# Kernel optimization log

Hardware: AMD Instinct MI355X
Metric: run time of the kernel (lower is better)

Reference implementation:

```python
import math
import jax, jax.numpy as jnp
import numpy as np

B, L, D = 8, 4096, 512
FACTOR = 5


def setup_inputs() -> dict:
    key = jax.random.key(0)
    kq, kk, kv = jax.random.split(key, 3)
    q = jax.random.normal(kq, (B, L, D), dtype=jnp.float32)
    k = jax.random.normal(kk, (B, L, D), dtype=jnp.float32)
    v = jax.random.normal(kv, (B, L, D), dtype=jnp.float32)
    return {"q": q, "k": k, "v": v}


def reference(q, k, v):
    # ProbSparse attention (sparse=True branch, L_Q > 1)
    L_Q = q.shape[1]
    scale = q.shape[-1] ** -0.5
    # scores: [B, L_Q, L_K]
    scores = jnp.einsum('bqd,bkd->bqk', q, k) * scale
    # sparsity measure M = max - mean over keys: [B, L_Q]
    M = scores.max(axis=-1) - scores.mean(axis=-1)
    u = max(1, int(FACTOR * math.log(L_Q + 1)))
    u = min(u, L_Q)  # static python int (u = 41 here)
    _, top_idx = jax.lax.top_k(M, u)  # [B, u]
    # gather top-u query rows of scores, softmax over keys (row-wise softmax
    # commutes with row selection, so this matches softmax-then-gather)
    scores_top = jnp.take_along_axis(scores, top_idx[:, :, None], axis=1)  # [B, u, L_K]
    attn = jax.nn.softmax(scores_top, axis=-1)
    out_top = jnp.einsum('buk,bkd->bud', attn, v)  # [B, u, D]
    # non-selected queries receive the mean value
    v_mean = jnp.broadcast_to(v.mean(axis=1, keepdims=True), v.shape)  # [B, L, D]
    b_idx = jnp.arange(q.shape[0])[:, None]  # [B, 1]
    out = v_mean.at[b_idx, top_idx].set(out_top)
    return out
```

## Files before the change

kernel.cpp:

```cpp
#include <hip/hip_runtime.h>
#include <math.h>

#define B_ 8
#define L_ 4096
#define D_ 512
#define U_ 41
#define NSL 16

static constexpr float SCALE = 0.044194173824159216f;

typedef __attribute__((ext_vector_type(8))) short bf16x8;
typedef __attribute__((ext_vector_type(4))) float f32x4;
typedef unsigned int uint;


__global__ __launch_bounds__(512) void kSums1(const float* __restrict__ k,
                                              const float* __restrict__ v,
                                              float* __restrict__ partk,
                                              float* __restrict__ partv) {
  const int s = blockIdx.x;
  const int b = blockIdx.y;
  const int d = threadIdx.x;
  const int rows = L_ / NSL;
  const size_t base = ((size_t)b * L_ + (size_t)s * rows) * D_ + d;
  float ks = 0.f, vs = 0.f;
  for (int l = 0; l < rows; ++l) {
    ks += k[base + (size_t)l * D_];
    vs += v[base + (size_t)l * D_];
  }
  partk[(b * NSL + s) * D_ + d] = ks;
  partv[(b * NSL + s) * D_ + d] = vs;
}

__global__ __launch_bounds__(512) void kSums2(const float* __restrict__ partk,
                                              const float* __restrict__ partv,
                                              float* __restrict__ ksum,
                                              float* __restrict__ vmean) {
  const int b = blockIdx.x;
  const int d = threadIdx.x;
  float ks = 0.f, vs = 0.f;
  for (int s = 0; s < NSL; ++s) {
    ks += partk[(b * NSL + s) * D_ + d];
    vs += partv[(b * NSL + s) * D_ + d];
  }
  ksum[b * D_ + d] = ks;
  vmean[b * D_ + d] = vs * (1.f / L_);
}

__global__ __launch_bounds__(256) void kMeanM(const float* __restrict__ q,
                                              const float* __restrict__ ksum,
                                              const float* __restrict__ pmax,
                                              float* __restrict__ M) {
  __shared__ float ks[D_];
  const int gid = blockIdx.x * 256 + threadIdx.x;
  const int b = gid >> 12;
  for (int i = threadIdx.x; i < D_; i += 256) ks[i] = ksum[b * D_ + i];
  __syncthreads();
  const float* qp = q + (size_t)gid * D_;
  float acc = 0.f;
  for (int i = 0; i < D_; i += 4) {
    float4 t = *(const float4*)(qp + i);
    acc += t.x * ks[i] + t.y * ks[i + 1] + t.z * ks[i + 2] + t.w * ks[i + 3];
  }
  const float rowmax = fmaxf(pmax[gid], pmax[B_ * L_ + gid]);
  M[gid] = SCALE * (rowmax - acc * (1.f / L_));
}

__global__ __launch_bounds__(256) void kTopK3(const float* __restrict__ M,
                                              int* __restrict__ topidx) {
  __shared__ float wv[2][4];
  __shared__ int wi[2][4];
  const int b = blockIdx.x;
  const int tid = threadIdx.x;
  const int wave = tid >> 6, lane = tid & 63;
  float v[16];
#pragma unroll
  for (int j = 0; j < 16; ++j) v[j] = M[b * L_ + tid + j * 256];
  float bv = v[0];
  int bj = 0;
#pragma unroll
  for (int j = 1; j < 16; ++j)
    if (v[j] > bv) { bv = v[j]; bj = j; }
  int bi = tid + bj * 256;

  for (int it = 0; it < U_; ++it) {
    float rv = bv;
    int ri = bi;
#pragma unroll
    for (int off = 1; off < 64; off <<= 1) {
      float ov = __shfl_xor(rv, off);
      int oi = __shfl_xor(ri, off);
      if (ov > rv || (ov == rv && oi < ri)) { rv = ov; ri = oi; }
    }
    const int par = it & 1;
    if (lane == 0) { wv[par][wave] = rv; wi[par][wave] = ri; }
    __syncthreads();
    float gv = wv[par][0];
    int gi = wi[par][0];
#pragma unroll
    for (int w = 1; w < 4; ++w) {
      float ov = wv[par][w];
      int oi = wi[par][w];
      if (ov > gv || (ov == gv && oi < gi)) { gv = ov; gi = oi; }
    }
    if (tid == 0) topidx[b * U_ + it] = gi;
    if (gi == bi) {
      const int jb = gi >> 8;
#pragma unroll
      for (int j = 0; j < 16; ++j)
        if (j == jb) v[j] = -3.4e38f;
      bv = v[0];
      bj = 0;
#pragma unroll
      for (int j = 1; j < 16; ++j)
        if (v[j] > bv) { bv = v[j]; bj = j; }
      bi = tid + bj * 256;
    }
  }
}

__global__ __launch_bounds__(256) void kFill(const float* __restrict__ vmean,
                                             float* __restrict__ out) {
  const int g = blockIdx.x * 256 + threadIdx.x;
  const int d4 = g & 127;
  const int bl = g >> 7;
  const int b = bl >> 12;
  ((float4*)out)[g] = ((const float4*)vmean)[b * 128 + d4];
}

__device__ inline uint bf16_rne_bits(float x) {
  uint u = __builtin_bit_cast(uint, x);
  return (u + 0x7FFFu + ((u >> 16) & 1u)) >> 16;
}
__device__ inline float bits_to_f32(uint hi16) {
  return __builtin_bit_cast(float, hi16 << 16);
}

__global__ __launch_bounds__(256) void kConvert(const float* __restrict__ src,
                                                unsigned char* __restrict__ dhi,
                                                unsigned char* __restrict__ dlo) {
  const int cid = blockIdx.x * 256 + threadIdx.x;
  const int c16 = cid & 7;
  const int row = (cid >> 3) & 127;
  const int dsi = (cid >> 10) & 7;
  const int rt = (cid >> 13) & 31;
  const int b = cid >> 18;
  const int l = rt * 128 + row;
  const int d = dsi * 64 + c16 * 8;
  const float* sp = src + ((size_t)(b * L_ + l) * D_ + d);
  float x[8];
  *(float4*)(x) = *(const float4*)sp;
  *(float4*)(x + 4) = *(const float4*)(sp + 4);
  uint hw[4], lw[4];
#pragma unroll
  for (int p = 0; p < 4; ++p) {
    float a = x[2 * p], c = x[2 * p + 1];
    uint ha = bf16_rne_bits(a), hc = bf16_rne_bits(c);
    float ra = a - bits_to_f32(ha);
    float rc = c - bits_to_f32(hc);
    uint la = bf16_rne_bits(ra), lc = bf16_rne_bits(rc);
    hw[p] = ha | (hc << 16);
    lw[p] = la | (lc << 16);
  }
  const size_t dstByte = ((size_t)(cid >> 3) << 7) +
                         (uint)((c16 << 4) ^ ((row & 7) << 4));
  *(uint4*)(dhi + dstByte) = make_uint4(hw[0], hw[1], hw[2], hw[3]);
  *(uint4*)(dlo + dstByte) = make_uint4(lw[0], lw[1], lw[2], lw[3]);
}

__device__ __forceinline__ void gload16(const unsigned char* g, unsigned char* l) {
  __builtin_amdgcn_global_load_lds(
      (const __attribute__((address_space(1))) unsigned int*)(g),
      (__attribute__((address_space(3))) unsigned int*)(l), 16, 0, 0);
}

__global__ __launch_bounds__(256, 1) void kRowMaxC(const unsigned char* __restrict__ qhi,
                                                   const unsigned char* __restrict__ qlo,
                                                   const unsigned char* __restrict__ khi,
                                                   const unsigned char* __restrict__ klo,
                                                   float* __restrict__ pmax) {
  __shared__ unsigned char lds[131072];

  const int wg = blockIdx.x;
  const int swz = (wg & 7) * 64 + (wg >> 3);
  const int qt = swz & 31;
  const int b = (swz >> 5) & 7;
  const int kh = swz >> 8;

  const int tid = threadIdx.x;
  const int lane = tid & 63;
  const int wave = tid >> 6;
  const int wq = wave >> 1, wk = wave & 1;

  const unsigned char* qhB = qhi + ((size_t)((b * 32 + qt) * 8)) * 16384;
  const unsigned char* qlB = qlo + ((size_t)((b * 32 + qt) * 8)) * 16384;
  const size_t kbase = ((size_t)((b * 32 + kh * 16) * 8)) * 16384;
  const unsigned char* khB = khi + kbase;
  const unsigned char* klB = klo + kbase;

  const size_t lof = (size_t)tid * 16;

  auto STAGE = [&](int s, unsigned char* buf) {
    const int dsi = s & 7;
    const size_t qof = (size_t)dsi * 16384 + lof;
    const size_t kof = (size_t)s * 16384 + lof;
#pragma unroll
    for (int i = 0; i < 4; ++i) {
      gload16(qhB + qof + i * 4096, buf + lof + i * 4096);
      gload16(qlB + qof + i * 4096, buf + 16384 + lof + i * 4096);
      gload16(khB + kof + i * 4096, buf + 32768 + lof + i * 4096);
      gload16(klB + kof + i * 4096, buf + 49152 + lof + i * 4096);
    }
  };

  float rmax[4][4];
  f32x4 acc[4][4];
#pragma unroll
  for (int i = 0; i < 4; ++i)
#pragma unroll
    for (int j = 0; j < 4; ++j) {
      rmax[i][j] = -3.4e38f;
#pragma unroll
      for (int e = 0; e < 4; ++e) acc[i][j][e] = 0.f;
    }

  auto PHASE = [&](int s, const unsigned char* bufR, unsigned char* bufW) {
    __syncthreads();
    if (s < 127) STAGE(s + 1, bufW);
#pragma unroll
    for (int h = 0; h < 2; ++h) {
      const int rbyte = h * 64 + ((lane >> 4) << 4);
      bf16x8 aH[4], aL[4], bH[4], bL[4];
#pragma unroll
      for (int f = 0; f < 4; ++f) {
        const int qrow = wq * 64 + f * 16 + (lane & 15);
        const int krow = wk * 64 + f * 16 + (lane & 15);
        const int qoff = qrow * 128 + (rbyte ^ ((qrow & 7) << 4));
        const int koff = krow * 128 + (rbyte ^ ((krow & 7) << 4));
        aH[f] = *(const bf16x8*)(bufR + qoff);
        aL[f] = *(const bf16x8*)(bufR + 16384 + qoff);
        bH[f] = *(const bf16x8*)(bufR + 32768 + koff);
        bL[f] = *(const bf16x8*)(bufR + 49152 + koff);
      }
#pragma unroll
      for (int mf = 0; mf < 4; ++mf)
#pragma unroll
        for (int nf = 0; nf < 4; ++nf) {
          acc[mf][nf] = __builtin_amdgcn_mfma_f32_16x16x32_bf16(aH[mf], bH[nf], acc[mf][nf], 0, 0, 0);
          acc[mf][nf] = __builtin_amdgcn_mfma_f32_16x16x32_bf16(aH[mf], bL[nf], acc[mf][nf], 0, 0, 0);
          acc[mf][nf] = __builtin_amdgcn_mfma_f32_16x16x32_bf16(aL[mf], bH[nf], acc[mf][nf], 0, 0, 0);
        }
    }
    if ((s & 7) == 7) {
#pragma unroll
      for (int mf = 0; mf < 4; ++mf)
#pragma unroll
        for (int r = 0; r < 4; ++r) {
          float m = fmaxf(fmaxf(acc[mf][0][r], acc[mf][1][r]),
                          fmaxf(acc[mf][2][r], acc[mf][3][r]));
          rmax[mf][r] = fmaxf(rmax[mf][r], m);
#pragma unroll
          for (int nf = 0; nf < 4; ++nf) acc[mf][nf][r] = 0.f;
        }
    }
  };

  STAGE(0, lds);
  for (int s = 0; s < 128; s += 2) {
    PHASE(s, lds, lds + 65536);
    PHASE(s + 1, lds + 65536, lds);
  }

#pragma unroll
  for (int mf = 0; mf < 4; ++mf)
#pragma unroll
    for (int r = 0; r < 4; ++r) {
      float v = rmax[mf][r];
#pragma unroll
      for (int off = 1; off < 16; off <<= 1) v = fmaxf(v, __shfl_xor(v, off));
      rmax[mf][r] = v;
    }

  __syncthreads();
  float* red = (float*)lds;
  if ((lane & 15) == 0) {
#pragma unroll
    for (int mf = 0; mf < 4; ++mf)
#pragma unroll
      for (int r = 0; r < 4; ++r) {
        const int rowl = wq * 64 + mf * 16 + ((lane >> 4) << 2) + r;
        red[wk * 128 + rowl] = rmax[mf][r];
      }
  }
  __syncthreads();
  if (tid < 128) {
    pmax[(size_t)kh * B_ * L_ + (size_t)b * L_ + qt * 128 + tid] =
        fmaxf(red[tid], red[128 + tid]);
  }
}


__global__ __launch_bounds__(64) void kGatherQ(const float* __restrict__ q,
                                               const int* __restrict__ topidx,
                                               unsigned char* __restrict__ qselhi,
                                               unsigned char* __restrict__ qsello) {
  const int j = blockIdx.x;
  const int b = blockIdx.y;
  const int lane = threadIdx.x;
  const int dsi = lane >> 3;
  const int c16 = lane & 7;
  float x[8] = {0.f, 0.f, 0.f, 0.f, 0.f, 0.f, 0.f, 0.f};
  if (j < U_) {
    const int row = topidx[b * U_ + j];
    const float* sp = q + ((size_t)(b * L_ + row)) * D_ + dsi * 64 + c16 * 8;
    *(float4*)(x) = *(const float4*)sp;
    *(float4*)(x + 4) = *(const float4*)(sp + 4);
  }
  uint hw[4], lw[4];
#pragma unroll
  for (int p = 0; p < 4; ++p) {
    float a = x[2 * p], c = x[2 * p + 1];
    uint ha = bf16_rne_bits(a), hc = bf16_rne_bits(c);
    float ra = a - bits_to_f32(ha);
    float rc = c - bits_to_f32(hc);
    uint la = bf16_rne_bits(ra), lc = bf16_rne_bits(rc);
    hw[p] = ha | (hc << 16);
    lw[p] = la | (lc << 16);
  }
  const size_t dstByte = ((size_t)((b * 8 + dsi) * 64 + j)) * 128 +
                         (uint)((c16 << 4) ^ ((j & 7) << 4));
  *(uint4*)(qselhi + dstByte) = make_uint4(hw[0], hw[1], hw[2], hw[3]);
  *(uint4*)(qsello + dstByte) = make_uint4(lw[0], lw[1], lw[2], lw[3]);
}

__global__ __launch_bounds__(256) void kSelScoresM(const unsigned char* __restrict__ qselhi,
                                                   const unsigned char* __restrict__ qsello,
                                                   const unsigned char* __restrict__ khi,
                                                   const unsigned char* __restrict__ klo,
                                                   float* __restrict__ P) {
  __shared__ unsigned char lds[49152];
  unsigned char* ldsQhi = lds;
  unsigned char* ldsQlo = lds + 8192;
  unsigned char* ldsKhi = lds + 16384;
  unsigned char* ldsKlo = lds + 32768;

  const int kc = blockIdx.x;
  const int b = blockIdx.y;
  const int tid = threadIdx.x;
  const int lane = tid & 63;
  const int wave = tid >> 6;
  const int wq = wave >> 1, wk = wave & 1;

  const size_t ktb = ((size_t)((b * 32 + kc) * 8)) * 16384;
  const unsigned char* khB = khi + ktb;
  const unsigned char* klB = klo + ktb;
  const size_t qb = ((size_t)b * 8) * 8192;
  const unsigned char* qhB = qselhi + qb;
  const unsigned char* qlB = qsello + qb;

  f32x4 acc[2][4];
#pragma unroll
  for (int i = 0; i < 2; ++i)
#pragma unroll
    for (int j = 0; j < 4; ++j)
#pragma unroll
      for (int e = 0; e < 4; ++e) acc[i][j][e] = 0.f;

  for (int dsi = 0; dsi < 8; ++dsi) {
    __syncthreads();
    {
      const size_t qof = (size_t)dsi * 8192 + (size_t)tid * 16;
      const size_t kof = (size_t)dsi * 16384 + (size_t)tid * 16;
      const size_t lof = (size_t)tid * 16;
#pragma unroll
      for (int i = 0; i < 2; ++i) {
        gload16(qhB + qof + i * 4096, ldsQhi + lof + i * 4096);
        gload16(qlB + qof + i * 4096, ldsQlo + lof + i * 4096);
      }
#pragma unroll
      for (int i = 0; i < 4; ++i) {
        gload16(khB + kof + i * 4096, ldsKhi + lof + i * 4096);
        gload16(klB + kof + i * 4096, ldsKlo + lof + i * 4096);
      }
    }
    __syncthreads();

#pragma unroll
    for (int h = 0; h < 2; ++h) {
      const int rbyte = h * 64 + ((lane >> 4) << 4);
      bf16x8 aH[2], aL[2], bH[4], bL[4];
#pragma unroll
      for (int f = 0; f < 2; ++f) {
        const int qrow = wq * 32 + f * 16 + (lane & 15);
        const int qoff = qrow * 128 + (rbyte ^ ((qrow & 7) << 4));
        aH[f] = *(const bf16x8*)(ldsQhi + qoff);
        aL[f] = *(const bf16x8*)(ldsQlo + qoff);
      }
#pragma unroll
      for (int f = 0; f < 4; ++f) {
        const int krow = wk * 64 + f * 16 + (lane & 15);
        const int koff = krow * 128 + (rbyte ^ ((krow & 7) << 4));
        bH[f] = *(const bf16x8*)(ldsKhi + koff);
        bL[f] = *(const bf16x8*)(ldsKlo + koff);
      }
#pragma unroll
      for (int mf = 0; mf < 2; ++mf)
#pragma unroll
        for (int nf = 0; nf < 4; ++nf) {
          acc[mf][nf] = __builtin_amdgcn_mfma_f32_16x16x32_bf16(aH[mf], bH[nf], acc[mf][nf], 0, 0, 0);
          acc[mf][nf] = __builtin_amdgcn_mfma_f32_16x16x32_bf16(aH[mf], bL[nf], acc[mf][nf], 0, 0, 0);
          acc[mf][nf] = __builtin_amdgcn_mfma_f32_16x16x32_bf16(aL[mf], bH[nf], acc[mf][nf], 0, 0, 0);
        }
    }
  }

#pragma unroll
  for (int mf = 0; mf < 2; ++mf)
#pragma unroll
    for (int nf = 0; nf < 4; ++nf)
#pragma unroll
      for (int r = 0; r < 4; ++r) {
        const int row = wq * 32 + mf * 16 + ((lane >> 4) << 2) + r;
        const int key = kc * 128 + wk * 64 + nf * 16 + (lane & 15);
        if (row < U_)
          P[((size_t)(b * U_ + row)) * L_ + key] = acc[mf][nf][r];
      }
}

__global__ __launch_bounds__(256) void kSoftmaxP(float* __restrict__ P) {
  __shared__ float red[256];
  const int j = blockIdx.x, b = blockIdx.y;
  float* row = P + ((size_t)(b * U_ + j)) * L_;
  const int tid = threadIdx.x;
  float v[16];
  float mx = -3.4e38f;
#pragma unroll
  for (int i = 0; i < 16; ++i) {
    v[i] = row[tid + i * 256];
    mx = fmaxf(mx, v[i]);
  }
  red[tid] = mx;
  __syncthreads();
  for (int s = 128; s > 0; s >>= 1) {
    if (tid < s) red[tid] = fmaxf(red[tid], red[tid + s]);
    __syncthreads();
  }
  mx = red[0];
  __syncthreads();
  float sum = 0.f;
#pragma unroll
  for (int i = 0; i < 16; ++i) {
    float e = expf((v[i] - mx) * SCALE);
    v[i] = e;
    sum += e;
  }
  red[tid] = sum;
  __syncthreads();
  for (int s = 128; s > 0; s >>= 1) {
    if (tid < s) red[tid] += red[tid + s];
    __syncthreads();
  }
  const float inv = 1.f / red[0];
#pragma unroll
  for (int i = 0; i < 16; ++i) row[tid + i * 256] = v[i] * inv;
}

__global__ __launch_bounds__(256) void kPV(const float* __restrict__ P,
                                           const float* __restrict__ v,
                                           float* __restrict__ partial) {
  __shared__ float plds[41 * 128];
  const int kc = blockIdx.x;
  const int dc = blockIdx.y;
  const int b = blockIdx.z;
  const int tid = threadIdx.x;
  const int trow = tid >> 7, dcol = tid & 127;
  float acc[U_];
#pragma unroll
  for (int j = 0; j < U_; ++j) acc[j] = 0.f;

  for (int sub = 0; sub < 4; ++sub) {
    const int key0 = kc * 512 + sub * 128;
    __syncthreads();
    for (int idx = tid; idx < U_ * 128; idx += 256)
      plds[idx] = P[((size_t)(b * U_ + (idx >> 7))) * L_ + key0 + (idx & 127)];
    __syncthreads();
    const float* vp = v + ((size_t)(b * L_ + key0 + trow * 64)) * D_ + dc * 128 + dcol;
    float vv[64];
#pragma unroll
    for (int kk = 0; kk < 64; ++kk) vv[kk] = vp[(size_t)kk * D_];
#pragma unroll
    for (int j = 0; j < U_; ++j) {
      const float4* pr = (const float4*)&plds[j * 128 + trow * 64];
      float a = acc[j];
#pragma unroll
      for (int q4 = 0; q4 < 16; ++q4) {
        float4 p4 = pr[q4];
        a = fmaf(p4.x, vv[q4 * 4 + 0], a);
        a = fmaf(p4.y, vv[q4 * 4 + 1], a);
        a = fmaf(p4.z, vv[q4 * 4 + 2], a);
        a = fmaf(p4.w, vv[q4 * 4 + 3], a);
      }
      acc[j] = a;
    }
  }
  float* pp = partial + ((size_t)((b * 4 + dc) * 16 + kc * 2 + trow)) * (U_ * 128) + dcol;
#pragma unroll
  for (int j = 0; j < U_; ++j) pp[j * 128] = acc[j];
}

__global__ __launch_bounds__(256) void kPVout(const float* __restrict__ partial,
                                              const int* __restrict__ topidx,
                                              float* __restrict__ out) {
  const int j = blockIdx.x, b = blockIdx.y;
  const int tid = threadIdx.x;
  const int l = topidx[b * U_ + j];
#pragma unroll
  for (int h = 0; h < 2; ++h) {
    const int d = tid + h * 256;
    const int dc = d >> 7, dcol = d & 127;
    float s = 0.f;
#pragma unroll
    for (int part = 0; part < 16; ++part)
      s += partial[((size_t)((b * 4 + dc) * 16 + part)) * (U_ * 128) + j * 128 + dcol];
    out[((size_t)(b * L_ + l)) * D_ + d] = s;
  }
}


__device__ inline void stageHalfRow(const float* __restrict__ src,
                                    char* hiBase, char* loBase,
                                    int row, int shalf) {
  const int sw = (row & 7) << 4;
  char* hp = hiBase + row * 128;
  char* lp = loBase + row * 128;
#pragma unroll
  for (int g = 0; g < 4; ++g) {
    f32x4 x0 = *(const f32x4*)(src + g * 8);
    f32x4 x1 = *(const f32x4*)(src + g * 8 + 4);
    float x[8] = {x0.x, x0.y, x0.z, x0.w, x1.x, x1.y, x1.z, x1.w};
    uint hw[4], lw[4];
#pragma unroll
    for (int p = 0; p < 4; ++p) {
      float a = x[2 * p], c = x[2 * p + 1];
      uint ha = bf16_rne_bits(a), hc = bf16_rne_bits(c);
      float ra = a - bits_to_f32(ha);
      float rc = c - bits_to_f32(hc);
      uint la = bf16_rne_bits(ra), lc = bf16_rne_bits(rc);
      hw[p] = ha | (hc << 16);
      lw[p] = la | (lc << 16);
    }
    const int off = (shalf * 64 + g * 16) ^ sw;
    *(uint4*)(hp + off) = make_uint4(hw[0], hw[1], hw[2], hw[3]);
    *(uint4*)(lp + off) = make_uint4(lw[0], lw[1], lw[2], lw[3]);
  }
}

__global__ __launch_bounds__(256, 2) void kRowMaxM(const float* __restrict__ q,
                                                   const float* __restrict__ k,
                                                   float* __restrict__ pmax) {
  __shared__ char lds[65536];
  __shared__ float red[256];
  char* ldsQhi = lds;
  char* ldsQlo = lds + 16384;
  char* ldsKhi = lds + 32768;
  char* ldsKlo = lds + 49152;

  const int b = blockIdx.y;
  const int qbase = blockIdx.x * 128;
  const int kh = blockIdx.z;
  const int tid = threadIdx.x;
  const int lane = tid & 63;
  const int wave = tid >> 6;
  const int wq = wave >> 1, wk = wave & 1;
  const int srow = tid >> 1;
  const int shalf = tid & 1;

  const float* qrow_base = q + ((size_t)b * L_ + qbase + srow) * D_ + shalf * 32;
  const float* krow_base = k + ((size_t)b * L_ + kh * 2048 + srow) * D_ + shalf * 32;

  float rmax[4][4];
#pragma unroll
  for (int i = 0; i < 4; ++i)
#pragma unroll
    for (int j = 0; j < 4; ++j) rmax[i][j] = -3.4e38f;

  for (int kt = 0; kt < 16; ++kt) {
    f32x4 acc[4][4];
#pragma unroll
    for (int i = 0; i < 4; ++i)
#pragma unroll
      for (int j = 0; j < 4; ++j)
#pragma unroll
        for (int e = 0; e < 4; ++e) acc[i][j][e] = 0.f;

    for (int dsi = 0; dsi < 8; ++dsi) {
      __syncthreads();
      stageHalfRow(qrow_base + dsi * 64, ldsQhi, ldsQlo, srow, shalf);
      stageHalfRow(krow_base + (size_t)kt * 128 * D_ + dsi * 64, ldsKhi, ldsKlo, srow, shalf);
      __syncthreads();

#pragma unroll
      for (int h = 0; h < 2; ++h) {
        const int rbyte = h * 64 + ((lane >> 4) << 4);
        bf16x8 aH[4], aL[4], bH[4], bL[4];
#pragma unroll
        for (int f = 0; f < 4; ++f) {
          const int qrow = wq * 64 + f * 16 + (lane & 15);
          const int krow = wk * 64 + f * 16 + (lane & 15);
          const int qoff = qrow * 128 + (rbyte ^ ((qrow & 7) << 4));
          const int koff = krow * 128 + (rbyte ^ ((krow & 7) << 4));
          aH[f] = *(const bf16x8*)(ldsQhi + qoff);
          aL[f] = *(const bf16x8*)(ldsQlo + qoff);
          bH[f] = *(const bf16x8*)(ldsKhi + koff);
          bL[f] = *(const bf16x8*)(ldsKlo + koff);
        }
#pragma unroll
        for (int mf = 0; mf < 4; ++mf)
#pragma unroll
          for (int nf = 0; nf < 4; ++nf) {
            acc[mf][nf] = __builtin_amdgcn_mfma_f32_16x16x32_bf16(aH[mf], bH[nf], acc[mf][nf], 0, 0, 0);
            acc[mf][nf] = __builtin_amdgcn_mfma_f32_16x16x32_bf16(aH[mf], bL[nf], acc[mf][nf], 0, 0, 0);
            acc[mf][nf] = __builtin_amdgcn_mfma_f32_16x16x32_bf16(aL[mf], bH[nf], acc[mf][nf], 0, 0, 0);
          }
      }
    }
#pragma unroll
    for (int mf = 0; mf < 4; ++mf)
#pragma unroll
      for (int r = 0; r < 4; ++r) {
        float m = fmaxf(fmaxf(acc[mf][0][r], acc[mf][1][r]),
                        fmaxf(acc[mf][2][r], acc[mf][3][r]));
        rmax[mf][r] = fmaxf(rmax[mf][r], m);
      }
  }

#pragma unroll
  for (int mf = 0; mf < 4; ++mf)
#pragma unroll
    for (int r = 0; r < 4; ++r) {
      float v = rmax[mf][r];
#pragma unroll
      for (int off = 1; off < 16; off <<= 1) v = fmaxf(v, __shfl_xor(v, off));
      rmax[mf][r] = v;
    }

  if ((lane & 15) == 0) {
#pragma unroll
    for (int mf = 0; mf < 4; ++mf)
#pragma unroll
      for (int r = 0; r < 4; ++r) {
        const int rowl = wq * 64 + mf * 16 + ((lane >> 4) << 2) + r;
        red[wk * 128 + rowl] = rmax[mf][r];
      }
  }
  __syncthreads();
  if (tid < 128) {
    pmax[(size_t)kh * B_ * L_ + (size_t)b * L_ + qbase + tid] =
        fmaxf(red[tid], red[128 + tid]);
  }
}

__global__ __launch_bounds__(256) void kAttnSel(const float* __restrict__ q,
                                                const float* __restrict__ k,
                                                const float* __restrict__ v,
                                                const int* __restrict__ topidx,
                                                float* __restrict__ out) {
  __shared__ float qs[D_];
  __shared__ float sc[L_];
  __shared__ float wred[4];
  __shared__ float sred[256];
  const int b = blockIdx.y;
  const int l_sel = topidx[b * U_ + blockIdx.x];
  const int tid = threadIdx.x;
  const int wave = tid >> 6, lane = tid & 63;
  const float* qrow = q + ((size_t)b * L_ + l_sel) * D_;
  qs[tid] = qrow[tid];
  qs[tid + 256] = qrow[tid + 256];
  __syncthreads();
  float qr[8];
#pragma unroll
  for (int i = 0; i < 8; ++i) qr[i] = qs[lane * 8 + i];
  float wmax = -3.4e38f;
  for (int l = wave; l < L_; l += 4) {
    const float* kp = k + ((size_t)b * L_ + l) * D_ + lane * 8;
    float4 k0 = *(const float4*)kp;
    float4 k1 = *(const float4*)(kp + 4);
    float p = k0.x * qr[0] + k0.y * qr[1] + k0.z * qr[2] + k0.w * qr[3] +
              k1.x * qr[4] + k1.y * qr[5] + k1.z * qr[6] + k1.w * qr[7];
#pragma unroll
    for (int off = 32; off > 0; off >>= 1) p += __shfl_xor(p, off);
    if (lane == 0) sc[l] = p;
    wmax = fmaxf(wmax, p);
  }
  if (lane == 0) wred[wave] = wmax;
  __syncthreads();
  const float mx = fmaxf(fmaxf(wred[0], wred[1]), fmaxf(wred[2], wred[3]));
  float psum = 0.f;
  for (int i = tid; i < L_; i += 256) {
    float e = expf((sc[i] - mx) * SCALE);
    sc[i] = e;
    psum += e;
  }
  sred[tid] = psum;
  __syncthreads();
  for (int s = 128; s > 0; s >>= 1) {
    if (tid < s) sred[tid] += sred[tid + s];
    __syncthreads();
  }
  const float inv = 1.f / sred[0];
  float a0a = 0.f, a0b = 0.f, a1a = 0.f, a1b = 0.f;
  const float* vb = v + (size_t)b * L_ * D_;
  for (int l = 0; l < L_; l += 2) {
    float p0 = sc[l], p1 = sc[l + 1];
    const float* vp0 = vb + (size_t)l * D_;
    const float* vp1 = vp0 + D_;
    a0a = fmaf(p0, vp0[tid], a0a);
    a1a = fmaf(p0, vp0[tid + 256], a1a);
    a0b = fmaf(p1, vp1[tid], a0b);
    a1b = fmaf(p1, vp1[tid + 256], a1b);
  }
  float* orow = out + ((size_t)b * L_ + l_sel) * D_;
  orow[tid] = (a0a + a0b) * inv;
  orow[tid + 256] = (a1a + a1b) * inv;
}


extern "C" void kernel_launch(void* const* d_in, const int* in_sizes, int n_in,
                              void* d_out, int out_size, void* d_ws, size_t ws_size,
                              hipStream_t stream) {
  const float* q = (const float*)d_in[0];
  const float* k = (const float*)d_in[1];
  const float* v = (const float*)d_in[2];
  float* out = (float*)d_out;
  unsigned char* wsb = (unsigned char*)d_ws;

  const size_t NEED = 84183040;

  if (ws_size >= NEED) {
    unsigned char* qhiW = wsb;
    unsigned char* qloW = wsb + 33554432;
    float* pmax = (float*)(wsb + 67108864);
    float* Marr = (float*)(wsb + 67371008);
    float* ksum = (float*)(wsb + 67502080);
    float* vmean = (float*)(wsb + 67518464);
    int* tidx = (int*)(wsb + 67534848);
    float* partk = (float*)(wsb + 67536896);
    float* partv = (float*)(wsb + 67799040);
    float* P = (float*)(wsb + 68061184);
    float* partial = (float*)(wsb + 73435136);
    unsigned char* qselhi = (unsigned char*)partial;
    unsigned char* qsello = qselhi + 524288;
    unsigned char* khiO = (unsigned char*)d_out;
    unsigned char* kloO = khiO + 33554432;

    kConvert<<<8192, 256, 0, stream>>>(q, qhiW, qloW);
    kConvert<<<8192, 256, 0, stream>>>(k, khiO, kloO);
    kSums1<<<dim3(NSL, B_), 512, 0, stream>>>(k, v, partk, partv);
    kSums2<<<B_, 512, 0, stream>>>(partk, partv, ksum, vmean);
    kRowMaxC<<<512, 256, 0, stream>>>(qhiW, qloW, khiO, kloO, pmax);
    kMeanM<<<B_ * L_ / 256, 256, 0, stream>>>(q, ksum, pmax, Marr);
    kTopK3<<<B_, 256, 0, stream>>>(Marr, tidx);
    kGatherQ<<<dim3(64, B_), 64, 0, stream>>>(q, tidx, qselhi, qsello);
    kSelScoresM<<<dim3(32, B_), 256, 0, stream>>>(qselhi, qsello, khiO, kloO, P);
    kSoftmaxP<<<dim3(U_, B_), 256, 0, stream>>>(P);
    kFill<<<B_ * L_ * D_ / 1024, 256, 0, stream>>>(vmean, out);
    kPV<<<dim3(8, 4, B_), 256, 0, stream>>>(P, v, partial);
    kPVout<<<dim3(U_, B_), 256, 0, stream>>>(partial, tidx, out);
  } else {
    float* ws = (float*)d_ws;
    float* Marr = ws;
    float* pmax = ws + 32768;
    float* ksum = ws + 98304;
    float* vmean = ws + 102400;
    int* tidx = (int*)(ws + 106496);
    float* partk = ws + 107008;
    float* partv = ws + 107008 + B_ * NSL * D_;

    kSums1<<<dim3(NSL, B_), 512, 0, stream>>>(k, v, partk, partv);
    kSums2<<<B_, 512, 0, stream>>>(partk, partv, ksum, vmean);
    kRowMaxM<<<dim3(L_ / 128, B_, 2), 256, 0, stream>>>(q, k, pmax);
    kMeanM<<<B_ * L_ / 256, 256, 0, stream>>>(q, ksum, pmax, Marr);
    kTopK3<<<B_, 256, 0, stream>>>(Marr, tidx);
    kFill<<<B_ * L_ * D_ / 1024, 256, 0, stream>>>(vmean, out);
    kAttnSel<<<dim3(U_, B_), 256, 0, stream>>>(q, k, v, tidx, out);
  }
}
```

Before: 677.7 us.

## Fuse q·ksum into q conversion, fold M into top-k, restructure rowmax kernel

Computes the per-row q·ksum dot product inside the q bf16 split conversion, so the separate mean-score kernel no longer re-reads q. The M = max − mean computation moves into a new top-k kernel that reads pmax and qdot directly. The rowmax GEMM is restructured to reuse one 64KB LDS stage per d-slice with launch_bounds of 2 blocks per CU, replacing the double-buffered 128KB pipeline. This trades the load/compute overlap for higher occupancy. It also doubles the k/v sum slice count and compacts the workspace layout.

```diff
diff --git a/kernel.cpp b/kernel.cpp
--- a/kernel.cpp
+++ b/kernel.cpp
@@ -5,7 +5,7 @@
 #define L_ 4096
 #define D_ 512
 #define U_ 41
-#define NSL 16
+#define NSL 32
 
 static constexpr float SCALE = 0.044194173824159216f;
 
@@ -76,6 +76,63 @@
   float v[16];
 #pragma unroll
   for (int j = 0; j < 16; ++j) v[j] = M[b * L_ + tid + j * 256];
+  float bv = v[0];
+  int bj = 0;
+#pragma unroll
+  for (int j = 1; j < 16; ++j)
+    if (v[j] > bv) { bv = v[j]; bj = j; }
+  int bi = tid + bj * 256;
+
+  for (int it = 0; it < U_; ++it) {
+    float rv = bv;
+    int ri = bi;
+#pragma unroll
+    for (int off = 1; off < 64; off <<= 1) {
+      float ov = __shfl_xor(rv, off);
+      int oi = __shfl_xor(ri, off);
+      if (ov > rv || (ov == rv && oi < ri)) { rv = ov; ri = oi; }
+    }
+    const int par = it & 1;
+    if (lane == 0) { wv[par][wave] = rv; wi[par][wave] = ri; }
+    __syncthreads();
+    float gv = wv[par][0];
+    int gi = wi[par][0];
+#pragma unroll
+    for (int w = 1; w < 4; ++w) {
+      float ov = wv[par][w];
+      int oi = wi[par][w];
+      if (ov > gv || (ov == gv && oi < gi)) { gv = ov; gi = oi; }
+    }
+    if (tid == 0) topidx[b * U_ + it] = gi;
+    if (gi == bi) {
+      const int jb = gi >> 8;
+#pragma unroll
+      for (int j = 0; j < 16; ++j)
+        if (j == jb) v[j] = -3.4e38f;
+      bv = v[0];
+      bj = 0;
+#pragma unroll
+      for (int j = 1; j < 16; ++j)
+        if (v[j] > bv) { bv = v[j]; bj = j; }
+      bi = tid + bj * 256;
+    }
+  }
+}
+
+__global__ __launch_bounds__(256) void kTopK3M(const float* __restrict__ pmax,
+                                               const float* __restrict__ qdot,
+                                               int* __restrict__ topidx) {
+  __shared__ float wv[2][4];
+  __shared__ int wi[2][4];
+  const int b = blockIdx.x;
+  const int tid = threadIdx.x;
+  const int wave = tid >> 6, lane = tid & 63;
+  float v[16];
+#pragma unroll
+  for (int j = 0; j < 16; ++j) {
+    const int gid = b * L_ + tid + j * 256;
+    v[j] = SCALE * (fmaxf(pmax[gid], pmax[B_ * L_ + gid]) - qdot[gid] * (1.f / L_));
+  }
   float bv = v[0];
   int bj = 0;
 #pragma unroll
@@ -168,18 +225,76 @@
   *(uint4*)(dlo + dstByte) = make_uint4(lw[0], lw[1], lw[2], lw[3]);
 }
 
+__global__ __launch_bounds__(256) void kConvertQdot(const float* __restrict__ src,
+                                                    const float* __restrict__ ksum,
+                                                    unsigned char* __restrict__ dhi,
+                                                    unsigned char* __restrict__ dlo,
+                                                    float* __restrict__ qdot) {
+  const int cid = blockIdx.x * 256 + threadIdx.x;
+  const int c16 = cid & 7;
+  const int row = (cid >> 3) & 127;
+  const int dsi = (cid >> 10) & 7;
+  const int rt = (cid >> 13) & 31;
+  const int b = cid >> 18;
+  const int l = rt * 128 + row;
+  const int d = dsi * 64 + c16 * 8;
+  const float* sp = src + ((size_t)(b * L_ + l) * D_ + d);
+  float x[8];
+  *(float4*)(x) = *(const float4*)sp;
+  *(float4*)(x + 4) = *(const float4*)(sp + 4);
+
+  const float* kp = ksum + b * D_ + d;
+  float dot = 0.f;
+#pragma unroll
+  for (int i = 0; i < 8; ++i) dot += x[i] * kp[i];
+#pragma unroll
+  for (int off = 1; off < 8; off <<= 1) dot += __shfl_xor(dot, off);
+
+  uint hw[4], lw[4];
+#pragma unroll
+  for (int p = 0; p < 4; ++p) {
+    float a = x[2 * p], c = x[2 * p + 1];
+    uint ha = bf16_rne_bits(a), hc = bf16_rne_bits(c);
+    float ra = a - bits_to_f32(ha);
+    float rc = c - bits_to_f32(hc);
+    uint la = bf16_rne_bits(ra), lc = bf16_rne_bits(rc);
+    hw[p] = ha | (hc << 16);
+    lw[p] = la | (lc << 16);
+  }
+  const size_t dstByte = ((size_t)(cid >> 3) << 7) +
+                         (uint)((c16 << 4) ^ ((row & 7) << 4));
+  *(uint4*)(dhi + dstByte) = make_uint4(hw[0], hw[1], hw[2], hw[3]);
+  *(uint4*)(dlo + dstByte) = make_uint4(lw[0], lw[1], lw[2], lw[3]);
+  if (c16 == 0)
+    qdot[((size_t)dsi * B_ * L_) + b * L_ + l] = dot;
+}
+
+__global__ __launch_bounds__(256) void kQdotReduce(const float* __restrict__ qdotp,
+                                                   float* __restrict__ qdot) {
+  const int gid = blockIdx.x * 256 + threadIdx.x;
+  float s = 0.f;
+#pragma unroll
+  for (int i = 0; i < 8; ++i) s += qdotp[(size_t)i * B_ * L_ + gid];
+  qdot[gid] = s;
+}
+
 __device__ __forceinline__ void gload16(const unsigned char* g, unsigned char* l) {
   __builtin_amdgcn_global_load_lds(
       (const __attribute__((address_space(1))) unsigned int*)(g),
       (__attribute__((address_space(3))) unsigned int*)(l), 16, 0, 0);
 }
 
-__global__ __launch_bounds__(256, 1) void kRowMaxC(const unsigned char* __restrict__ qhi,
+__global__ __launch_bounds__(256, 2) void kRowMaxB(const unsigned char* __restrict__ qhi,
                                                    const unsigned char* __restrict__ qlo,
                                                    const unsigned char* __restrict__ khi,
                                                    const unsigned char* __restrict__ klo,
                                                    float* __restrict__ pmax) {
-  __shared__ unsigned char lds[131072];
+  __shared__ unsigned char lds[65536];
+  __shared__ float red[256];
+  unsigned char* ldsQhi = lds;
+  unsigned char* ldsQlo = lds + 16384;
+  unsigned char* ldsKhi = lds + 32768;
+  unsigned char* ldsKlo = lds + 49152;
 
   const int wg = blockIdx.x;
   const int swz = (wg & 7) * 64 + (wg >> 3);
@@ -192,83 +307,77 @@
   const int wave = tid >> 6;
   const int wq = wave >> 1, wk = wave & 1;
 
-  const unsigned char* qhB = qhi + ((size_t)((b * 32 + qt) * 8)) * 16384;
-  const unsigned char* qlB = qlo + ((size_t)((b * 32 + qt) * 8)) * 16384;
-  const size_t kbase = ((size_t)((b * 32 + kh * 16) * 8)) * 16384;
-  const unsigned char* khB = khi + kbase;
-  const unsigned char* klB = klo + kbase;
-
-  const size_t lof = (size_t)tid * 16;
-
-  auto STAGE = [&](int s, unsigned char* buf) {
-    const int dsi = s & 7;
-    const size_t qof = (size_t)dsi * 16384 + lof;
-    const size_t kof = (size_t)s * 16384 + lof;
-#pragma unroll
-    for (int i = 0; i < 4; ++i) {
-      gload16(qhB + qof + i * 4096, buf + lof + i * 4096);
-      gload16(qlB + qof + i * 4096, buf + 16384 + lof + i * 4096);
-      gload16(khB + kof + i * 4096, buf + 32768 + lof + i * 4096);
-      gload16(klB + kof + i * 4096, buf + 49152 + lof + i * 4096);
-    }
-  };
+  const size_t qtb = ((size_t)((b * 32 + qt) * 8)) * 16384;
+  const unsigned char* qhB = qhi + qtb;
+  const unsigned char* qlB = qlo + qtb;
 
   float rmax[4][4];
-  f32x4 acc[4][4];
 #pragma unroll
   for (int i = 0; i < 4; ++i)
 #pragma unroll
-    for (int j = 0; j < 4; ++j) {
-      rmax[i][j] = -3.4e38f;
-#pragma unroll
-      for (int e = 0; e < 4; ++e) acc[i][j][e] = 0.f;
-    }
-
-  auto PHASE = [&](int s, const unsigned char* bufR, unsigned char* bufW) {
-    __syncthreads();
-    if (s < 127) STAGE(s + 1, bufW);
-#pragma unroll
-    for (int h = 0; h < 2; ++h) {
-      const int rbyte = h * 64 + ((lane >> 4) << 4);
-      bf16x8 aH[4], aL[4], bH[4], bL[4];
-#pragma unroll
-      for (int f = 0; f < 4; ++f) {
-        const int qrow = wq * 64 + f * 16 + (lane & 15);
-        const int krow = wk * 64 + f * 16 + (lane & 15);
-        const int qoff = qrow * 128 + (rbyte ^ ((qrow & 7) << 4));
-        const int koff = krow * 128 + (rbyte ^ ((krow & 7) << 4));
-        aH[f] = *(const bf16x8*)(bufR + qoff);
-        aL[f] = *(const bf16x8*)(bufR + 16384 + qoff);
-        bH[f] = *(const bf16x8*)(bufR + 32768 + koff);
-        bL[f] = *(const bf16x8*)(bufR + 49152 + koff);
-      }
-#pragma unroll
-      for (int mf = 0; mf < 4; ++mf)
-#pragma unroll
-        for (int nf = 0; nf < 4; ++nf) {
-          acc[mf][nf] = __builtin_amdgcn_mfma_f32_16x16x32_bf16(aH[mf], bH[nf], acc[mf][nf], 0, 0, 0);
-          acc[mf][nf] = __builtin_amdgcn_mfma_f32_16x16x32_bf16(aH[mf], bL[nf], acc[mf][nf], 0, 0, 0);
-          acc[mf][nf] = __builtin_amdgcn_mfma_f32_16x16x32_bf16(aL[mf], bH[nf], acc[mf][nf], 0, 0, 0);
+    for (int j = 0; j < 4; ++j) rmax[i][j] = -3.4e38f;
+
+  for (int kt = 0; kt < 16; ++kt) {
+    const size_t ktb = ((size_t)((b * 32 + (kh * 16 + kt)) * 8)) * 16384;
+    const unsigned char* khB = khi + ktb;
+    const unsigned char* klB = klo + ktb;
+
+    f32x4 acc[4][4];
+#pragma unroll
+    for (int i = 0; i < 4; ++i)
+#pragma unroll
+      for (int j = 0; j < 4; ++j)
+#pragma unroll
+        for (int e = 0; e < 4; ++e) acc[i][j][e] = 0.f;
+
+    for (int dsi = 0; dsi < 8; ++dsi) {
+      __syncthreads();
+      {
+        const size_t dof = (size_t)dsi * 16384 + (size_t)tid * 16;
+        const size_t lof = (size_t)tid * 16;
+#pragma unroll
+        for (int i = 0; i < 4; ++i) {
+          gload16(qhB + dof + i * 4096, ldsQhi + lof + i * 4096);
+          gload16(qlB + dof + i * 4096, ldsQlo + lof + i * 4096);
+          gload16(khB + dof + i * 4096, ldsKhi + lof + i * 4096);
+          gload16(klB + dof + i * 4096, ldsKlo + lof + i * 4096);
         }
-    }
-    if ((s & 7) == 7) {
-#pragma unroll
-      for (int mf = 0; mf < 4; ++mf)
-#pragma unroll
-        for (int r = 0; r < 4; ++r) {
-          float m = fmaxf(fmaxf(acc[mf][0][r], acc[mf][1][r]),
-                          fmaxf(acc[mf][2][r], acc[mf][3][r]));
-          rmax[mf][r] = fmaxf(rmax[mf][r], m);
-#pragma unroll
-          for (int nf = 0; nf < 4; ++nf) acc[mf][nf][r] = 0.f;
+      }
+      __syncthreads();
+
+#pragma unroll
+      for (int h = 0; h < 2; ++h) {
+        const int rbyte = h * 64 + ((lane >> 4) << 4);
+        bf16x8 aH[4], aL[4], bH[4], bL[4];
+#pragma unroll
+        for (int f = 0; f < 4; ++f) {
+          const int qrow = wq * 64 + f * 16 + (lane & 15);
+          const int krow = wk * 64 + f * 16 + (lane & 15);
+          const int qoff = qrow * 128 + (rbyte ^ ((qrow & 7) << 4));
+          const int koff = krow * 128 + (rbyte ^ ((krow & 7) << 4));
+          aH[f] = *(const bf16x8*)(ldsQhi + qoff);
+          aL[f] = *(const bf16x8*)(ldsQlo + qoff);
+          bH[f] = *(const bf16x8*)(ldsKhi + koff);
+          bL[f] = *(const bf16x8*)(ldsKlo + koff);
         }
-    }
-  };
-
-  STAGE(0, lds);
-  for (int s = 0; s < 128; s += 2) {
-    PHASE(s, lds, lds + 65536);
-    PHASE(s + 1, lds + 65536, lds);
+#pragma unroll
+        for (int mf = 0; mf < 4; ++mf)
+#pragma unroll
+          for (int nf = 0; nf < 4; ++nf) {
+            acc[mf][nf] = __builtin_amdgcn_mfma_f32_16x16x32_bf16(aH[mf], bH[nf], acc[mf][nf], 0, 0, 0);
+            acc[mf][nf] = __builtin_amdgcn_mfma_f32_16x16x32_bf16(aH[mf], bL[nf], acc[mf][nf], 0, 0, 0);
+            acc[mf][nf] = __builtin_amdgcn_mfma_f32_16x16x32_bf16(aL[mf], bH[nf], acc[mf][nf], 0, 0, 0);
+          }
+      }
+    }
+#pragma unroll
+    for (int mf = 0; mf < 4; ++mf)
+#pragma unroll
+      for (int r = 0; r < 4; ++r) {
+        float m = fmaxf(fmaxf(acc[mf][0][r], acc[mf][1][r]),
+                        fmaxf(acc[mf][2][r], acc[mf][3][r]));
+        rmax[mf][r] = fmaxf(rmax[mf][r], m);
+      }
   }
 
 #pragma unroll
@@ -281,8 +390,6 @@
       rmax[mf][r] = v;
     }
 
-  __syncthreads();
-  float* red = (float*)lds;
   if ((lane & 15) == 0) {
 #pragma unroll
     for (int mf = 0; mf < 4; ++mf)
@@ -734,32 +841,34 @@
   float* out = (float*)d_out;
   unsigned char* wsb = (unsigned char*)d_ws;
 
-  const size_t NEED = 84183040;
+  const size_t NEED = 68585472;
 
   if (ws_size >= NEED) {
     unsigned char* qhiW = wsb;
     unsigned char* qloW = wsb + 33554432;
+    float* P = (float*)wsb;
+    float* partial = (float*)(wsb + 5373952);
+    unsigned char* qselhi = wsb + 16121856;
+    unsigned char* qsello = wsb + 16646144;
     float* pmax = (float*)(wsb + 67108864);
-    float* Marr = (float*)(wsb + 67371008);
+    float* qdot = (float*)(wsb + 67371008);
     float* ksum = (float*)(wsb + 67502080);
     float* vmean = (float*)(wsb + 67518464);
     int* tidx = (int*)(wsb + 67534848);
     float* partk = (float*)(wsb + 67536896);
-    float* partv = (float*)(wsb + 67799040);
-    float* P = (float*)(wsb + 68061184);
-    float* partial = (float*)(wsb + 73435136);
-    unsigned char* qselhi = (unsigned char*)partial;
-    unsigned char* qsello = qselhi + 524288;
+    float* partv = (float*)(wsb + 68061184);
+    float* qdotp = partk;
+
     unsigned char* khiO = (unsigned char*)d_out;
     unsigned char* kloO = khiO + 33554432;
 
-    kConvert<<<8192, 256, 0, stream>>>(q, qhiW, qloW);
-    kConvert<<<8192, 256, 0, stream>>>(k, khiO, kloO);
     kSums1<<<dim3(NSL, B_), 512, 0, stream>>>(k, v, partk, partv);
     kSums2<<<B_, 512, 0, stream>>>(partk, partv, ksum, vmean);
-    kRowMaxC<<<512, 256, 0, stream>>>(qhiW, qloW, khiO, kloO, pmax);
-    kMeanM<<<B_ * L_ / 256, 256, 0, stream>>>(q, ksum, pmax, Marr);
-    kTopK3<<<B_, 256, 0, stream>>>(Marr, tidx);
+    kConvertQdot<<<8192, 256, 0, stream>>>(q, ksum, qhiW, qloW, qdotp);
+    kQdotReduce<<<B_ * L_ / 256, 256, 0, stream>>>(qdotp, qdot);
+    kConvert<<<8192, 256, 0, stream>>>(k, khiO, kloO);
+    kRowMaxB<<<512, 256, 0, stream>>>(qhiW, qloW, khiO, kloO, pmax);
+    kTopK3M<<<B_, 256, 0, stream>>>(pmax, qdot, tidx);
     kGatherQ<<<dim3(64, B_), 64, 0, stream>>>(q, tidx, qselhi, qsello);
     kSelScoresM<<<dim3(32, B_), 256, 0, stream>>>(qselhi, qsello, khiO, kloO, P);
     kSoftmaxP<<<dim3(U_, B_), 256, 0, stream>>>(P);
```

Result: faster. 601.9 us (-11.2%).
